# Optimization experiments

Measured on AMD Instinct MI355X. Metric: run time of the kernel, lower is better.

## Reference

```python
import jax, jax.numpy as jnp
import numpy as np

TEMPERATURE = 0.5
F_EPS = 1e-12   # torch F.normalize default eps
COS_EPS = 1e-8  # torch cosine_similarity default eps


def setup_inputs() -> dict:
    key = jax.random.key(0)
    k1, k2, k3 = jax.random.split(key, 3)
    B, S, D, T = 64, 2048, 256, 64
    features = jax.random.normal(k1, (B, S, D), dtype=jnp.float32)
    labels = jax.random.randint(k2, (B, S), 0, T)
    label_emb = jax.random.normal(k3, (T, D), dtype=jnp.float32)  # nn.Embedding weight
    return {"features": features, "labels": labels, "label_emb": label_emb}


def reference(features, labels, label_emb):
    # features: [B, S, D], labels: [B, S] int, label_emb: [T, D]
    num_tags = label_emb.shape[0]
    mask = jax.nn.one_hot(labels, num_tags, dtype=features.dtype)  # [B, S, T]

    # F.normalize(features, p=2, dim=-1): x / max(||x||, eps)
    f = features / jnp.maximum(
        jnp.linalg.norm(features, axis=-1, keepdims=True), F_EPS)
    # cosine_similarity(proto, f): f already unit-norm, so only proto norm matters
    p = label_emb / jnp.maximum(
        jnp.linalg.norm(label_emb, axis=-1, keepdims=True), COS_EPS)

    # nested-loop get_att_dis == one batched matmul of unit vectors
    sim = jnp.einsum('bsd,td->bst', f, p)  # [B, S, T] cosine similarities

    inv_t = 1.0 / TEMPERATURE
    pos = jnp.sum(jnp.exp(sim * mask * inv_t) * mask, axis=-1)          # [B, S]
    neg_mask = 1.0 - mask
    neg = jnp.sum(jnp.exp(sim * neg_mask * inv_t) * neg_mask, axis=-1)  # [B, S]

    loss = -jnp.log(pos / neg)
    return loss.sum()
```

## Files before the change

### kernel.cpp

```cpp
#include <hip/hip_runtime.h>
#include <math.h>

typedef __attribute__((ext_vector_type(8))) short bf16x8;
typedef __attribute__((ext_vector_type(4))) float f32x4;

#define NTAGS 64

__device__ __forceinline__ short f2bf(float f) {
    unsigned u = __builtin_bit_cast(unsigned, f);
    u += 0x7fffu + ((u >> 16) & 1u);
    return (short)(u >> 16);
}

__global__ __launch_bounds__(256)
void lcl_prep(const float* __restrict__ lemb, bf16x8* __restrict__ ws)
{
    __shared__ float part[4][NTAGS];
    __shared__ float scl[NTAGS];
    const int tid = threadIdx.x;
    const float4* lemb4 = (const float4*)lemb;

    {
        int t = tid & 63, p = tid >> 6;
        float ss = 0.f;
        #pragma unroll
        for (int j = 0; j < 16; ++j) {
            float4 q = lemb4[t * 64 + p * 16 + j];
            ss += q.x*q.x + q.y*q.y + q.z*q.z + q.w*q.w;
        }
        part[p][t] = ss;
    }
    __syncthreads();
    if (tid < NTAGS) {
        float ss = part[0][tid] + part[1][tid] + part[2][tid] + part[3][tid];
        scl[tid] = 1.0f / fmaxf(sqrtf(ss), 1e-8f);
    }
    __syncthreads();

    const int e = blockIdx.x * 256 + tid;
    const int chunk = e >> 6, t = e & 63;
    const float s = scl[t];
    float4 q0 = lemb4[t * 64 + chunk * 2];
    float4 q1 = lemb4[t * 64 + chunk * 2 + 1];
    bf16x8 pk;
    pk[0] = f2bf(q0.x * s); pk[1] = f2bf(q0.y * s);
    pk[2] = f2bf(q0.z * s); pk[3] = f2bf(q0.w * s);
    pk[4] = f2bf(q1.x * s); pk[5] = f2bf(q1.y * s);
    pk[6] = f2bf(q1.z * s); pk[7] = f2bf(q1.w * s);
    ws[e] = pk;
}

__global__ __launch_bounds__(512, 4)
void lcl_main(const float* __restrict__ feat,
              const int*   __restrict__ labels,
              const bf16x8* __restrict__ protoWS,
              float*       __restrict__ blockPart)
{
    __shared__ bf16x8 protoB[2048];
    __shared__ float  wsum[8];
    const int tid = threadIdx.x;

    #pragma unroll
    for (int i = 0; i < 4; ++i)
        protoB[i * 512 + tid] = protoWS[i * 512 + tid];
    __syncthreads();

    const int lane = tid & 63;
    const int wv   = tid >> 6;
    const int g = lane >> 4;
    const int r = lane & 15;
    const int r0 = (blockIdx.x * 8 + wv) * 16;

    const float4* feat4 = (const float4*)feat;
    const size_t base = (size_t)(r0 + r) * 64 + g * 2;

    float4 q[16];
    #pragma unroll
    for (int ks = 0; ks < 8; ++ks) {
        q[2 * ks]     = feat4[base + ks * 8];
        q[2 * ks + 1] = feat4[base + ks * 8 + 1];
    }
    const int4 lb = ((const int4*)labels)[(r0 >> 2) + g];

    f32x4 acc[4];
    #pragma unroll
    for (int ct = 0; ct < 4; ++ct) acc[ct] = (f32x4){0.f, 0.f, 0.f, 0.f};

    float sq = 0.f;
    #pragma unroll
    for (int ks = 0; ks < 8; ++ks) {
        float4 q0 = q[2 * ks], q1 = q[2 * ks + 1];
        sq = fmaf(q0.x, q0.x, fmaf(q0.y, q0.y, fmaf(q0.z, q0.z, fmaf(q0.w, q0.w, sq))));
        sq = fmaf(q1.x, q1.x, fmaf(q1.y, q1.y, fmaf(q1.z, q1.z, fmaf(q1.w, q1.w, sq))));
        bf16x8 af;
        af[0] = f2bf(q0.x); af[1] = f2bf(q0.y);
        af[2] = f2bf(q0.z); af[3] = f2bf(q0.w);
        af[4] = f2bf(q1.x); af[5] = f2bf(q1.y);
        af[6] = f2bf(q1.z); af[7] = f2bf(q1.w);
        const int cbase = (ks * 4 + g) * 64;
        #pragma unroll
        for (int ct = 0; ct < 4; ++ct)
            acc[ct] = __builtin_amdgcn_mfma_f32_16x16x32_bf16(
                          af, protoB[cbase + ct * 16 + r], acc[ct], 0, 0, 0);
    }

    sq += __shfl_xor(sq, 16, 64);
    sq += __shfl_xor(sq, 32, 64);
    const float rn = 1.0f / fmaxf(sqrtf(sq), 1e-12f);

    float wloss = 0.f;
    #pragma unroll
    for (int reg = 0; reg < 4; ++reg) {
        const int rowi = g * 4 + reg;
        float rr  = __shfl(rn, rowi, 64);
        const int lbl = (reg == 0) ? lb.x : (reg == 1) ? lb.y : (reg == 2) ? lb.z : lb.w;
        float en = 0.f, pos = 0.f;
        #pragma unroll
        for (int ct = 0; ct < 4; ++ct) {
            float sim = acc[ct][reg] * rr;
            float e   = __expf(2.0f * sim);
            bool  m   = (lbl == ct * 16 + r);
            en  += m ? 0.f : e;
            pos += m ? 2.0f * sim : 0.f;
        }
        #pragma unroll
        for (int o = 1; o < 16; o <<= 1) {
            en  += __shfl_xor(en,  o, 64);
            pos += __shfl_xor(pos, o, 64);
        }
        wloss += __logf(en) - pos;
    }

    wloss += __shfl_xor(wloss, 16, 64);
    wloss += __shfl_xor(wloss, 32, 64);
    if (lane == 0) wsum[wv] = wloss;
    __syncthreads();
    if (tid == 0) {
        float b = wsum[0] + wsum[1] + wsum[2] + wsum[3]
                + wsum[4] + wsum[5] + wsum[6] + wsum[7];
        blockPart[blockIdx.x] = b;
    }
}

__global__ __launch_bounds__(256)
void lcl_reduce(const float* __restrict__ part, float* __restrict__ out)
{
    __shared__ float s[4];
    const int tid = threadIdx.x;
    float v = part[tid] + part[tid + 256] + part[tid + 512] + part[tid + 768];
    #pragma unroll
    for (int o = 1; o < 64; o <<= 1) v += __shfl_xor(v, o, 64);
    if ((tid & 63) == 0) s[tid >> 6] = v;
    __syncthreads();
    if (tid == 0) out[0] = s[0] + s[1] + s[2] + s[3];
}

extern "C" void kernel_launch(void* const* d_in, const int* in_sizes, int n_in,
                              void* d_out, int out_size, void* d_ws, size_t ws_size,
                              hipStream_t stream) {
    const float* feat   = (const float*)d_in[0];
    const int*   labels = (const int*)d_in[1];
    const float* lemb   = (const float*)d_in[2];
    float*       out    = (float*)d_out;
    bf16x8*      ws     = (bf16x8*)d_ws;
    float*       part   = (float*)((char*)d_ws + 32768);

    lcl_prep<<<8, 256, 0, stream>>>(lemb, ws);

    const int nrows = in_sizes[1];
    const int grid  = nrows / (8 * 16);
    lcl_main<<<grid, 512, 0, stream>>>(feat, labels, ws, part);
    lcl_reduce<<<1, 256, 0, stream>>>(part, out);
}
```

Before: 34.35 us.

## Fuse final reduction into main kernel via last-block atomic counter

Removes the separate reduction kernel launch. Each block publishes its partial sum with a release store and bumps an atomic counter, and the last block to arrive sums all partials and writes the output. The counter is reset in the prep kernel. The main kernel also issues its feature loads before writing the prototypes into LDS, so global loads overlap the shared-memory fill, and it splits the squared-norm accumulation into two chains. The cost is atomic traffic plus a tail reduction done inside the last block.

```diff
diff --git a/kernel.cpp b/kernel.cpp
--- a/kernel.cpp
+++ b/kernel.cpp
@@ -13,13 +13,15 @@
 }
 
 __global__ __launch_bounds__(256)
-void lcl_prep(const float* __restrict__ lemb, bf16x8* __restrict__ ws)
+void lcl_prep(const float* __restrict__ lemb, bf16x8* __restrict__ ws,
+              unsigned* __restrict__ counter)
 {
     __shared__ float part[4][NTAGS];
     __shared__ float scl[NTAGS];
     const int tid = threadIdx.x;
+    if (blockIdx.x == 0 && tid == 0)
+        __hip_atomic_store(counter, 0u, __ATOMIC_RELAXED, __HIP_MEMORY_SCOPE_AGENT);
     const float4* lemb4 = (const float4*)lemb;
-
     {
         int t = tid & 63, p = tid >> 6;
         float ss = 0.f;
@@ -36,7 +38,6 @@
         scl[tid] = 1.0f / fmaxf(sqrtf(ss), 1e-8f);
     }
     __syncthreads();
-
     const int e = blockIdx.x * 256 + tid;
     const int chunk = e >> 6, t = e & 63;
     const float s = scl[t];
@@ -54,26 +55,26 @@
 void lcl_main(const float* __restrict__ feat,
               const int*   __restrict__ labels,
               const bf16x8* __restrict__ protoWS,
-              float*       __restrict__ blockPart)
+              float*       __restrict__ blockPart,
+              unsigned*    __restrict__ counter,
+              float*       __restrict__ out)
 {
     __shared__ bf16x8 protoB[2048];
     __shared__ float  wsum[8];
-    const int tid = threadIdx.x;
-
-    #pragma unroll
-    for (int i = 0; i < 4; ++i)
-        protoB[i * 512 + tid] = protoWS[i * 512 + tid];
-    __syncthreads();
-
+    __shared__ int    lastFlag;
+    const int tid  = threadIdx.x;
     const int lane = tid & 63;
     const int wv   = tid >> 6;
     const int g = lane >> 4;
     const int r = lane & 15;
     const int r0 = (blockIdx.x * 8 + wv) * 16;
+    const float4* feat4 = (const float4*)feat;
 
-    const float4* feat4 = (const float4*)feat;
+    bf16x8 pw[4];
+    #pragma unroll
+    for (int i = 0; i < 4; ++i) pw[i] = protoWS[i * 512 + tid];
+
     const size_t base = (size_t)(r0 + r) * 64 + g * 2;
-
     float4 q[16];
     #pragma unroll
     for (int ks = 0; ks < 8; ++ks) {
@@ -82,16 +83,24 @@
     }
     const int4 lb = ((const int4*)labels)[(r0 >> 2) + g];
 
+    #pragma unroll
+    for (int i = 0; i < 4; ++i) protoB[i * 512 + tid] = pw[i];
+
+    #pragma unroll
+    for (int i = 0; i < 16; ++i)
+        asm volatile("" :: "v"(q[i].x), "v"(q[i].y), "v"(q[i].z), "v"(q[i].w));
+    __syncthreads();
+
     f32x4 acc[4];
     #pragma unroll
     for (int ct = 0; ct < 4; ++ct) acc[ct] = (f32x4){0.f, 0.f, 0.f, 0.f};
 
-    float sq = 0.f;
+    float sqa = 0.f, sqb = 0.f;
     #pragma unroll
     for (int ks = 0; ks < 8; ++ks) {
         float4 q0 = q[2 * ks], q1 = q[2 * ks + 1];
-        sq = fmaf(q0.x, q0.x, fmaf(q0.y, q0.y, fmaf(q0.z, q0.z, fmaf(q0.w, q0.w, sq))));
-        sq = fmaf(q1.x, q1.x, fmaf(q1.y, q1.y, fmaf(q1.z, q1.z, fmaf(q1.w, q1.w, sq))));
+        sqa = fmaf(q0.x, q0.x, fmaf(q0.y, q0.y, fmaf(q0.z, q0.z, fmaf(q0.w, q0.w, sqa))));
+        sqb = fmaf(q1.x, q1.x, fmaf(q1.y, q1.y, fmaf(q1.z, q1.z, fmaf(q1.w, q1.w, sqb))));
         bf16x8 af;
         af[0] = f2bf(q0.x); af[1] = f2bf(q0.y);
         af[2] = f2bf(q0.z); af[3] = f2bf(q0.w);
@@ -104,6 +113,7 @@
                           af, protoB[cbase + ct * 16 + r], acc[ct], 0, 0, 0);
     }
 
+    float sq = sqa + sqb;
     sq += __shfl_xor(sq, 16, 64);
     sq += __shfl_xor(sq, 32, 64);
     const float rn = 1.0f / fmaxf(sqrtf(sq), 1e-12f);
@@ -138,21 +148,26 @@
     if (tid == 0) {
         float b = wsum[0] + wsum[1] + wsum[2] + wsum[3]
                 + wsum[4] + wsum[5] + wsum[6] + wsum[7];
-        blockPart[blockIdx.x] = b;
+        __hip_atomic_store(&blockPart[blockIdx.x], b,
+                           __ATOMIC_RELEASE, __HIP_MEMORY_SCOPE_AGENT);
+        unsigned old = __hip_atomic_fetch_add(counter, 1u,
+                           __ATOMIC_ACQ_REL, __HIP_MEMORY_SCOPE_AGENT);
+        lastFlag = (old == gridDim.x - 1) ? 1 : 0;
     }
-}
-
-__global__ __launch_bounds__(256)
-void lcl_reduce(const float* __restrict__ part, float* __restrict__ out)
-{
-    __shared__ float s[4];
-    const int tid = threadIdx.x;
-    float v = part[tid] + part[tid + 256] + part[tid + 512] + part[tid + 768];
-    #pragma unroll
-    for (int o = 1; o < 64; o <<= 1) v += __shfl_xor(v, o, 64);
-    if ((tid & 63) == 0) s[tid >> 6] = v;
     __syncthreads();
-    if (tid == 0) out[0] = s[0] + s[1] + s[2] + s[3];
+    if (lastFlag) {
+        float v = __hip_atomic_load(&blockPart[tid],
+                      __ATOMIC_ACQUIRE, __HIP_MEMORY_SCOPE_AGENT)
+                + __hip_atomic_load(&blockPart[tid + 512],
+                      __ATOMIC_ACQUIRE, __HIP_MEMORY_SCOPE_AGENT);
+        #pragma unroll
+        for (int o = 1; o < 64; o <<= 1) v += __shfl_xor(v, o, 64);
+        if (lane == 0) wsum[wv] = v;
+        __syncthreads();
+        if (tid == 0)
+            out[0] = wsum[0] + wsum[1] + wsum[2] + wsum[3]
+                   + wsum[4] + wsum[5] + wsum[6] + wsum[7];
+    }
 }
 
 extern "C" void kernel_launch(void* const* d_in, const int* in_sizes, int n_in,
@@ -164,11 +179,11 @@
     float*       out    = (float*)d_out;
     bf16x8*      ws     = (bf16x8*)d_ws;
     float*       part   = (float*)((char*)d_ws + 32768);
+    unsigned*    counter= (unsigned*)((char*)d_ws + 36864);
 
-    lcl_prep<<<8, 256, 0, stream>>>(lemb, ws);
+    lcl_prep<<<8, 256, 0, stream>>>(lemb, ws, counter);
 
     const int nrows = in_sizes[1];
     const int grid  = nrows / (8 * 16);
-    lcl_main<<<grid, 512, 0, stream>>>(feat, labels, ws, part);
-    lcl_reduce<<<1, 256, 0, stream>>>(part, out);
+    lcl_main<<<grid, 512, 0, stream>>>(feat, labels, ws, part, counter, out);
 }
```

After: 66.52 us. 1.94x slower.
